# Performance work log

Hardware: AMD Instinct MI355X
Metric: run time of the kernel (lower is better)

## Reference

```python
import jax, jax.numpy as jnp
import numpy as np

NL = 2    # num_layers
H = 4     # attention heads
C = 512   # hidden_dim
IN = 256  # in_dim
F = 16    # fanout
B = 256   # seed nodes
NC = 47   # num_classes
DH = C // H
EPS = 1e-5


def _ln(x, g, b):
    mu = jnp.mean(x, -1, keepdims=True)
    var = jnp.mean((x - mu) ** 2, -1, keepdims=True)
    return (x - mu) * jax.lax.rsqrt(var + EPS) * g + b


def _mha(x, wqkv, bqkv, wo, bo):
    # torch nn.MultiheadAttention with a single batch of N tokens
    n = x.shape[0]
    qkv = x @ wqkv.T + bqkv                      # [N, 3C]
    q, k, v = jnp.split(qkv, 3, axis=-1)
    q = q.reshape(n, H, DH).transpose(1, 0, 2)   # [H, N, DH]
    k = k.reshape(n, H, DH).transpose(1, 0, 2)
    v = v.reshape(n, H, DH).transpose(1, 0, 2)
    s = jnp.einsum('hnd,hmd->hnm', q, k) * (1.0 / float(np.sqrt(DH)))
    a = jax.nn.softmax(s, axis=-1)
    o = jnp.einsum('hnm,hmd->hnd', a, v).transpose(1, 0, 2).reshape(n, C)
    return o @ wo.T + bo


def setup_inputs() -> dict:
    ks = jax.random.split(jax.random.key(0), 16)
    n = [B, B * F, B * F * F]
    p = lambda i, shape: jax.random.normal(ks[i], shape, jnp.float32) * 0.02
    return {
        'feats0': jax.random.normal(ks[0], (n[0], IN), jnp.float32),
        'feats1': jax.random.normal(ks[1], (n[1], IN), jnp.float32),
        'feats2': jax.random.normal(ks[2], (n[2], IN), jnp.float32),
        'nmask0': jnp.ones((n[0],), jnp.float32),
        'nmask1': jnp.ones((n[1],), jnp.float32),
        'nmask2': jnp.ones((n[2],), jnp.float32),
        'nbmask0': jax.random.randint(ks[3], (n[0], F), 0, 2, jnp.int32),
        'nbmask1': jax.random.randint(ks[4], (n[1], F), 0, 2, jnp.int32),
        'emb_w': p(5, (C, IN)), 'emb_b': jnp.zeros((C,), jnp.float32),
        'sage_w': p(6, (NL, C, 2 * C)), 'sage_b': jnp.zeros((NL, C), jnp.float32),
        'qkv_w': p(7, (NL, 3 * C, C)), 'qkv_b': jnp.zeros((NL, 3 * C), jnp.float32),
        'out_w': p(8, (NL, C, C)), 'out_b': jnp.zeros((NL, C), jnp.float32),
        'n1_g': jnp.ones((NL, C), jnp.float32), 'n1_b': jnp.zeros((NL, C), jnp.float32),
        'n2_g': jnp.ones((NL, C), jnp.float32), 'n2_b': jnp.zeros((NL, C), jnp.float32),
        'ffn_w1': p(9, (NL, 2 * C, C)), 'ffn_b1': jnp.zeros((NL, 2 * C), jnp.float32),
        'ffn_w2': p(10, (NL, C, 2 * C)), 'ffn_b2': jnp.zeros((NL, C), jnp.float32),
        'cls_w': p(11, (NC, C)), 'cls_b': jnp.zeros((NC,), jnp.float32),
    }


def reference(feats0, feats1, feats2, nmask0, nmask1, nmask2, nbmask0, nbmask1,
              emb_w, emb_b, sage_w, sage_b, qkv_w, qkv_b, out_w, out_b,
              n1_g, n1_b, n2_g, n2_b, ffn_w1, ffn_b1, ffn_w2, ffn_b2, cls_w, cls_b):
    nmasks = [nmask0, nmask1, nmask2]
    nbm = [nbmask0.astype(jnp.float32), nbmask1.astype(jnp.float32)]
    # embedding + node-mask gating per depth
    states = [(f @ emb_w.T + emb_b) * m[:, None]
              for f, m in zip([feats0, feats1, feats2], nmasks)]
    for li in range(NL):
        prev = states
        nxt = list(prev)
        for depth in range(NL - li - 1, -1, -1):
            # masked mean aggregation of sampled neighbors: [n_d, F, C] -> [n_d, C]
            child = prev[depth + 1].reshape(-1, F, C)
            m = nbm[depth][:, :, None]
            summed = jnp.sum(child * m, axis=1)
            denom = jnp.clip(jnp.sum(m, axis=1), 1.0)
            agg = summed / denom
            sf = prev[depth]
            # GraphSAGE concat update (no activation, dropout=0)
            h_local = jnp.concatenate([sf, agg], -1) @ sage_w[li].T + sage_b[li]
            h = _ln(sf + h_local, n1_g[li], n1_b[li])
            h = _ln(h + _mha(h, qkv_w[li], qkv_b[li], out_w[li], out_b[li]),
                    n2_g[li], n2_b[li])
            hf = jax.nn.relu(h @ ffn_w1[li].T + ffn_b1[li]) @ ffn_w2[li].T + ffn_b2[li]
            nxt[depth] = (h + hf) * nmasks[depth][:, None]
        states = nxt
    return states[0] @ cls_w.T + cls_b
```

## Files before the change

kernel.cpp:

```cpp
#include <hip/hip_runtime.h>
#include <math.h>


typedef unsigned short bf16_t;
typedef __attribute__((ext_vector_type(8))) short bf16x8_t;
typedef __attribute__((ext_vector_type(4))) float f32x4_t;

#define M_BIG 4096
#define M_CAT 4352
#define NSPLIT 4

__device__ __forceinline__ bf16_t f2bf(float f) {
  union { float f; unsigned u; } v; v.f = f;
  unsigned r = v.u + 0x7FFFu + ((v.u >> 16) & 1u);
  return (bf16_t)(r >> 16);
}
__device__ __forceinline__ float bf2f(bf16_t u) {
  union { unsigned u; float f; } v; v.u = ((unsigned)u) << 16; return v.f;
}
__device__ __forceinline__ unsigned cvtpk(float lo, float hi) {
  unsigned r;
  asm("v_cvt_pk_bf16_f32 %0, %1, %2" : "=v"(r) : "v"(lo), "v"(hi));
  return r;
}
__device__ __forceinline__ void gload16(const void* g, void* l) {
  __builtin_amdgcn_global_load_lds(
      (const __attribute__((address_space(1))) unsigned int*)g,
      (__attribute__((address_space(3))) unsigned int*)l, 16, 0, 0);
}

#define QSCALE (0.08838834764831845f * 1.4426950408889634f)

template <int BM, int BN, int MODE, bool SPLIT>
__global__ __launch_bounds__(256) void mgemm(
    const bf16_t* __restrict__ A, const bf16_t* __restrict__ A2,
    const bf16_t* __restrict__ W, const float* __restrict__ bias,
    const bf16_t* __restrict__ res, const float* __restrict__ rowa,
    const float* __restrict__ rowa2, const float* __restrict__ rowb,
    const float* __restrict__ rowc,
    bf16_t* __restrict__ Cb, bf16_t* __restrict__ Vt,
    int M, int M1, int N, int K) {
  constexpr int FM = BM / 32, FN = BN / 32;
  constexpr int NCH = (BM + BN) / 16;
  constexpr int CPW = NCH / 4;
  __shared__ bf16_t lds[2][(BM + BN) * 32];
  const int t = threadIdx.x;
  const int w = t >> 6, lane = t & 63;
  const int g = lane >> 4, li = lane & 15;
  const int bm = blockIdx.x * BM, bn = blockIdx.y * BN;
  const int wr = (w >> 1) * (BM / 2), wc = (w & 1) * (BN / 2);
  f32x4_t acc[FM][FN] = {};

  auto stage = [&](int buf, int k0) {
#pragma unroll
    for (int c0 = 0; c0 < CPW; ++c0) {
      const int c = w * CPW + c0;
      const int row = c * 16 + (lane >> 2);
      const int gk = k0 + (lane & 3) * 8;
      const bf16_t* src;
      if (row < BM) {
        const int grow = bm + row;
        if (MODE == 6) {
          src = (grow < M_CAT) ? (A + (size_t)grow * K + gk)
                               : (A2 + (size_t)(grow - M_CAT) * K + gk);
        } else if (SPLIT) {
          src = (gk < 512) ? (A + (size_t)grow * 512 + gk)
                           : (A2 + (size_t)grow * 512 + (gk - 512));
        } else {
          src = A + (size_t)grow * K + gk;
        }
      } else {
        src = W + (size_t)(bn + row - BM) * K + gk;
      }
      gload16(src, &lds[buf][c * 512]);
    }
  };

  const int nk = K / 32;
  stage(0, 0);
  for (int ks = 0; ks < nk; ++ks) {
    __syncthreads();
    if (ks + 1 < nk) stage((ks + 1) & 1, (ks + 1) * 32);
    const bf16_t* As = &lds[ks & 1][0];
    const bf16_t* Bs = &lds[ks & 1][BM * 32];
    bf16x8_t af[FM], bfr[FN];
#pragma unroll
    for (int i = 0; i < FM; ++i)
      af[i] = *(const bf16x8_t*)(As + (wr + i * 16 + li) * 32 + g * 8);
#pragma unroll
    for (int j = 0; j < FN; ++j)
      bfr[j] = *(const bf16x8_t*)(Bs + (wc + j * 16 + li) * 32 + g * 8);
#pragma unroll
    for (int i = 0; i < FM; ++i)
#pragma unroll
      for (int j = 0; j < FN; ++j)
        acc[i][j] = __builtin_amdgcn_mfma_f32_16x16x32_bf16(
            af[i], bfr[j], acc[i][j], 0, 0, 0);
  }

#pragma unroll
  for (int i = 0; i < FM; ++i) {
    const int mb = bm + wr + i * 16 + g * 4;
#pragma unroll
    for (int j = 0; j < FN; ++j) {
      const int n = bn + wc + j * 16 + li;
      if (MODE == 5) {
        const float bb = bias[n];
        if (n < 512) {
#pragma unroll
          for (int r = 0; r < 4; ++r)
            Cb[(size_t)(mb + r) * 1024 + n] = f2bf((acc[i][j][r] + bb) * QSCALE);
        } else if (n < 1024) {
#pragma unroll
          for (int r = 0; r < 4; ++r)
            Cb[(size_t)(mb + r) * 1024 + n] = f2bf(acc[i][j][r] + bb);
        } else {
          ushort4 o;
          o.x = f2bf(acc[i][j][0] + bb); o.y = f2bf(acc[i][j][1] + bb);
          o.z = f2bf(acc[i][j][2] + bb); o.w = f2bf(acc[i][j][3] + bb);
          *(ushort4*)(Vt + (size_t)(n - 1024) * M + mb) = o;
        }
      } else {
#pragma unroll
        for (int r = 0; r < 4; ++r) {
          const int m = mb + r;
          const float v = acc[i][j][r];
          if (MODE == 0) Cb[(size_t)m * N + n] = f2bf(v + bias[n]);
          if (MODE == 3) Cb[(size_t)m * N + n] = f2bf(fmaxf(v + bias[n], 0.f));
          if (MODE == 4) {
            const float ra = (m < M1) ? rowa[m] : rowa2[m - M1];
            Cb[(size_t)m * N + n] =
                f2bf((v + bias[n] + bf2f(res[(size_t)m * N + n])) * ra);
          }
          if (MODE == 6) {
            float val;
            if (m < M1) val = (v + bias[n]) * rowa[m];
            else if (m < M_CAT) val = (v + bias[n]) * rowa2[m - M1];
            else {
              const int mm = m - M_CAT;
              val = (v + bias[n] * rowb[mm]) * rowc[mm];
            }
            Cb[(size_t)m * N + n] = f2bf(val);
          }
        }
      }
    }
  }
}

template <int NW, int NQC, int SPLITS>
__global__ __launch_bounds__(NW * 64) void flashT(
    const bf16_t* __restrict__ qk, const bf16_t* __restrict__ vt,
    bf16_t* __restrict__ attno, bf16_t* __restrict__ Ofb,
    float* __restrict__ Ml, int N, int VS) {
  constexpr int QB = NW * NQC * 16;
  constexpr int KCH = 16 / NW;
  __shared__ bf16_t Ks[2][64 * 128];
  __shared__ bf16_t Vs[2][128 * 64];
  __shared__ bf16_t Ps[NW][16 * 64];
  const int bid = blockIdx.x;
  const int sp = bid % SPLITS;
  const int h = (bid / SPLITS) & 3;
  const int qb = bid / (4 * SPLITS);
  const int t = threadIdx.x, w = t >> 6, lane = t & 63;
  const int g = lane >> 4, li = lane & 15;
  const int kvbase = sp * (N / SPLITS);
  const int nt = (N / SPLITS) >> 6;

  bf16x8_t qf[NQC][4];
#pragma unroll
  for (int qc = 0; qc < NQC; ++qc) {
    const bf16_t* qrow =
        qk + (size_t)(qb * QB + w * (NQC * 16) + qc * 16 + li) * 1024 + h * 128;
#pragma unroll
    for (int ks = 0; ks < 4; ++ks)
      qf[qc][ks] = *(const bf16x8_t*)(qrow + ks * 32 + g * 8);
  }

  int koff[4], voff[2], pwoff[4];
#pragma unroll
  for (int ks = 0; ks < 4; ++ks)
    koff[ks] = li * 256 + (((ks * 4 + g) ^ (li & 7)) << 4);
#pragma unroll
  for (int ks = 0; ks < 2; ++ks)
    voff[ks] = li * 128 + (((ks * 4 + g) ^ (li & 7)) << 4);
#pragma unroll
  for (int mf = 0; mf < 4; ++mf)
    pwoff[mf] = li * 128 + (((mf * 2 + (g >> 1)) ^ (li & 7)) << 4) +
                ((g & 1) << 3);
  char* Pb = (char*)Ps + w * 2048;

  const bf16_t* kp[KCH];
  const bf16_t* vp[KCH];
#pragma unroll
  for (int i = 0; i < KCH; ++i) {
    const int c = w * KCH + i;
    const int rk = c * 4 + (lane >> 4);
    kp[i] = qk + (size_t)(kvbase + rk) * 1024 + 512 + h * 128 +
            (((lane & 15) ^ (rk & 7)) * 8);
    const int rv = c * 8 + (lane >> 3);
    vp[i] = vt + (size_t)(h * 128 + rv) * VS + kvbase +
            (((lane & 7) ^ (rv & 7)) * 8);
  }
  auto stage = [&](int buf) {
#pragma unroll
    for (int i = 0; i < KCH; ++i) {
      const int c = w * KCH + i;
      gload16(kp[i], &Ks[buf][c * 512]);
      kp[i] += (size_t)64 * 1024;
      gload16(vp[i], &Vs[buf][c * 512]);
      vp[i] += 64;
    }
  };

  f32x4_t acc[NQC][8] = {};
  float mrun[NQC], lrun[NQC];
#pragma unroll
  for (int qc = 0; qc < NQC; ++qc) { mrun[qc] = -1e30f; lrun[qc] = 0.f; }

  stage(0);
  for (int tt = 0; tt < nt; ++tt) {
    const int cur = tt & 1;
    __syncthreads();
    if (tt + 1 < nt) stage(cur ^ 1);
    const char* Kb = (const char*)Ks + cur * 16384;
    const char* Vb = (const char*)Vs + cur * 16384;

    f32x4_t sf[NQC][4];
#pragma unroll
    for (int qc = 0; qc < NQC; ++qc)
#pragma unroll
      for (int mf = 0; mf < 4; ++mf) sf[qc][mf] = (f32x4_t){0.f, 0.f, 0.f, 0.f};
    __builtin_amdgcn_s_setprio(1);
#pragma unroll
    for (int ks = 0; ks < 4; ++ks) {
#pragma unroll
      for (int mf = 0; mf < 4; ++mf) {
        const bf16x8_t kf = *(const bf16x8_t*)(Kb + koff[ks] + mf * 4096);
#pragma unroll
        for (int qc = 0; qc < NQC; ++qc)
          sf[qc][mf] = __builtin_amdgcn_mfma_f32_16x16x32_bf16(
              kf, qf[qc][ks], sf[qc][mf], 0, 0, 0);
      }
    }
    __builtin_amdgcn_s_setprio(0);

    float tmax[NQC];
#pragma unroll
    for (int qc = 0; qc < NQC; ++qc) {
      float tm = -1e30f;
#pragma unroll
      for (int mf = 0; mf < 4; ++mf)
#pragma unroll
        for (int r = 0; r < 4; ++r) tm = fmaxf(tm, sf[qc][mf][r]);
      tm = fmaxf(tm, __shfl_xor(tm, 16));
      tm = fmaxf(tm, __shfl_xor(tm, 32));
      tmax[qc] = tm;
    }
    float worst = tmax[0] - mrun[0];
#pragma unroll
    for (int qc = 1; qc < NQC; ++qc)
      worst = fmaxf(worst, tmax[qc] - mrun[qc]);
    if (!__all(worst <= 11.0f)) {
#pragma unroll
      for (int qc = 0; qc < NQC; ++qc) {
        const float mnew = fmaxf(mrun[qc], tmax[qc]);
        const float fsc = exp2f(mrun[qc] - mnew);
        mrun[qc] = mnew;
        lrun[qc] *= fsc;
#pragma unroll
        for (int mf = 0; mf < 8; ++mf) acc[qc][mf] *= fsc;
      }
    }
#pragma unroll
    for (int qc = 0; qc < NQC; ++qc) {
      float lsum = 0.f;
#pragma unroll
      for (int mf = 0; mf < 4; ++mf)
#pragma unroll
        for (int r = 0; r < 4; ++r) {
          const float p = exp2f(sf[qc][mf][r] - mrun[qc]);
          sf[qc][mf][r] = p;
          lsum += p;
        }
      lsum += __shfl_xor(lsum, 16);
      lsum += __shfl_xor(lsum, 32);
      lrun[qc] += lsum;
    }

    __builtin_amdgcn_s_setprio(1);
#pragma unroll
    for (int qc = 0; qc < NQC; ++qc) {
#pragma unroll
      for (int mf = 0; mf < 4; ++mf) {
        uint2 pv;
        pv.x = cvtpk(sf[qc][mf][0], sf[qc][mf][1]);
        pv.y = cvtpk(sf[qc][mf][2], sf[qc][mf][3]);
        *(uint2*)(Pb + pwoff[mf]) = pv;
      }
#pragma unroll
      for (int ks = 0; ks < 2; ++ks) {
        const bf16x8_t pf = *(const bf16x8_t*)(Pb + voff[ks]);
#pragma unroll
        for (int mf = 0; mf < 8; ++mf) {
          const bf16x8_t vf = *(const bf16x8_t*)(Vb + voff[ks] + mf * 2048);
          acc[qc][mf] = __builtin_amdgcn_mfma_f32_16x16x32_bf16(
              vf, pf, acc[qc][mf], 0, 0, 0);
        }
      }
    }
    __builtin_amdgcn_s_setprio(0);
  }

#pragma unroll
  for (int qc = 0; qc < NQC; ++qc) {
    const float invl = 1.f / lrun[qc];
    const int q = qb * QB + w * (NQC * 16) + qc * 16 + li;
    bf16_t* dst = (SPLITS == 1) ? (attno + (size_t)q * 512 + h * 128)
                                : (Ofb + ((size_t)sp * N + q) * 512 + h * 128);
#pragma unroll
    for (int mf = 0; mf < 8; ++mf) {
      ushort4 o;
      o.x = f2bf(acc[qc][mf][0] * invl); o.y = f2bf(acc[qc][mf][1] * invl);
      o.z = f2bf(acc[qc][mf][2] * invl); o.w = f2bf(acc[qc][mf][3] * invl);
      *(ushort4*)(dst + mf * 16 + g * 4) = o;
    }
    if (SPLITS > 1 && lane < 16) {
      float2 ml; ml.x = mrun[qc]; ml.y = lrun[qc];
      *(float2*)(Ml + ((size_t)(sp * 4 + h) * N + q) * 2) = ml;
    }
  }
}

template <int SPLITS>
__global__ __launch_bounds__(256) void merge_attn(
    const bf16_t* __restrict__ Ofb, const float* __restrict__ Ml,
    bf16_t* __restrict__ attno, int N) {
  const int q = blockIdx.x, t = threadIdx.x;
#pragma unroll
  for (int half = 0; half < 2; ++half) {
    const int c = t + half * 256;
    const int h = c >> 7;
    float2 ml[SPLITS];
    float m = -1e30f;
#pragma unroll
    for (int s = 0; s < SPLITS; ++s) {
      ml[s] = ((const float2*)Ml)[(s * 4 + h) * N + q];
      m = fmaxf(m, ml[s].x);
    }
    float num = 0.f, den = 0.f;
#pragma unroll
    for (int s = 0; s < SPLITS; ++s) {
      const float wgt = ml[s].y * exp2f(ml[s].x - m);
      num += bf2f(Ofb[((size_t)s * N + q) * 512 + c]) * wgt;
      den += wgt;
    }
    attno[(size_t)q * 512 + c] = f2bf(num / den);
  }
}

__global__ __launch_bounds__(256) void add_ln(
    const bf16_t* __restrict__ X, const bf16_t* __restrict__ Y,
    const float* __restrict__ gg, const float* __restrict__ bb,
    bf16_t* __restrict__ out) {
  const int row = blockIdx.x, t = threadIdx.x;
  const size_t base = (size_t)row * 512;
  const float x0 = bf2f(X[base + t]) + bf2f(Y[base + t]);
  const float x1 = bf2f(X[base + 256 + t]) + bf2f(Y[base + 256 + t]);
  float s = x0 + x1, ss = x0 * x0 + x1 * x1;
#pragma unroll
  for (int o = 32; o > 0; o >>= 1) {
    s += __shfl_down(s, o);
    ss += __shfl_down(ss, o);
  }
  __shared__ float rs[4], rss[4], sm[2];
  const int wv = t >> 6, ln = t & 63;
  if (ln == 0) { rs[wv] = s; rss[wv] = ss; }
  __syncthreads();
  if (t == 0) {
    const float S = rs[0] + rs[1] + rs[2] + rs[3];
    const float SS = rss[0] + rss[1] + rss[2] + rss[3];
    const float mean = S * (1.f / 512.f);
    sm[0] = mean;
    sm[1] = rsqrtf(SS * (1.f / 512.f) - mean * mean + 1e-5f);
  }
  __syncthreads();
  const float mean = sm[0], rstd = sm[1];
  out[base + t] = f2bf((x0 - mean) * rstd * gg[t] + bb[t]);
  out[base + 256 + t] = f2bf((x1 - mean) * rstd * gg[t + 256] + bb[t + 256]);
}

__global__ __launch_bounds__(256) void agg_feats(
    const float* __restrict__ feats2, const int* __restrict__ nbm,
    const float* __restrict__ nm2, bf16_t* __restrict__ aggF,
    float* __restrict__ sw, float* __restrict__ invd) {
  const int node = blockIdx.x * 4 + (threadIdx.x >> 6);
  const int lane = threadIdx.x & 63;
  float4 acc = {0.f, 0.f, 0.f, 0.f};
  float ws = 0.f, nbs = 0.f;
#pragma unroll
  for (int j = 0; j < 16; ++j) {
    const float nb = (float)nbm[node * 16 + j];
    const float wj = nb * nm2[node * 16 + j];
    const float4 v =
        *(const float4*)(feats2 + (size_t)(node * 16 + j) * 256 + lane * 4);
    acc.x += wj * v.x; acc.y += wj * v.y;
    acc.z += wj * v.z; acc.w += wj * v.w;
    ws += wj;
    nbs += nb;
  }
  ushort4 o;
  o.x = f2bf(acc.x); o.y = f2bf(acc.y); o.z = f2bf(acc.z); o.w = f2bf(acc.w);
  *(ushort4*)(aggF + (size_t)node * 256 + lane * 4) = o;
  if (lane == 0) { sw[node] = ws; invd[node] = 1.f / fmaxf(nbs, 1.f); }
}

__global__ __launch_bounds__(256) void agg_state(
    const bf16_t* __restrict__ src, const int* __restrict__ nbm,
    bf16_t* __restrict__ agg) {
  const int node = blockIdx.x * 4 + (threadIdx.x >> 6);
  const int lane = threadIdx.x & 63;
  float acc[8] = {};
  float nbs = 0.f;
#pragma unroll
  for (int j = 0; j < 16; ++j) {
    const float nb = (float)nbm[node * 16 + j];
    nbs += nb;
    const bf16x8_t v =
        *(const bf16x8_t*)(src + (size_t)(node * 16 + j) * 512 + lane * 8);
#pragma unroll
    for (int e = 0; e < 8; ++e) acc[e] += nb * bf2f((bf16_t)v[e]);
  }
  const float inv = 1.f / fmaxf(nbs, 1.f);
  bf16x8_t o;
#pragma unroll
  for (int e = 0; e < 8; ++e) o[e] = (short)f2bf(acc[e] * inv);
  *(bf16x8_t*)(agg + (size_t)node * 512 + lane * 8) = o;
}

__global__ __launch_bounds__(256) void cvt_all(
    const float* __restrict__ s_emb, const float* __restrict__ s_sage,
    const float* __restrict__ s_qkv, const float* __restrict__ s_out,
    const float* __restrict__ s_f1, const float* __restrict__ s_f2,
    const float* __restrict__ s_ft0, const float* __restrict__ s_ft1,
    bf16_t* __restrict__ d_emb, bf16_t* __restrict__ d_sage,
    bf16_t* __restrict__ d_qkv, bf16_t* __restrict__ d_out,
    bf16_t* __restrict__ d_f1, bf16_t* __restrict__ d_f2,
    bf16_t* __restrict__ d_ft0, bf16_t* __restrict__ d_ft1) {
  int i = blockIdx.x * 256 + threadIdx.x;
  const float* s; bf16_t* d; int base;
  if (i < 32768)        { s = s_emb;  d = d_emb;  base = 0; }
  else if (i < 294912)  { s = s_sage; d = d_sage; base = 32768; }
  else if (i < 688128)  { s = s_qkv;  d = d_qkv;  base = 294912; }
  else if (i < 819200)  { s = s_out;  d = d_out;  base = 688128; }
  else if (i < 1081344) { s = s_f1;   d = d_f1;   base = 819200; }
  else if (i < 1343488) { s = s_f2;   d = d_f2;   base = 1081344; }
  else if (i < 1359872) { s = s_ft0;  d = d_ft0;  base = 1343488; }
  else                  { s = s_ft1;  d = d_ft1;  base = 1359872; }
  i -= base;
  const float4 v = ((const float4*)s)[i];
  ushort4 o;
  o.x = f2bf(v.x); o.y = f2bf(v.y); o.z = f2bf(v.z); o.w = f2bf(v.w);
  ((ushort4*)d)[i] = o;
}

__global__ __launch_bounds__(256) void cls_k(
    const bf16_t* __restrict__ s, const float* __restrict__ wc,
    const float* __restrict__ bc, float* __restrict__ out) {
  __shared__ float srow[512];
  const int m = blockIdx.x, t = threadIdx.x;
  srow[t] = bf2f(s[(size_t)m * 512 + t]);
  srow[t + 256] = bf2f(s[(size_t)m * 512 + 256 + t]);
  __syncthreads();
  if (t < 47) {
    float a = bc[t];
    const float* wr = wc + (size_t)t * 512;
    for (int k = 0; k < 512; ++k) a += srow[k] * wr[k];
    out[(size_t)m * 47 + t] = a;
  }
}

extern "C" void kernel_launch(void* const* d_in, const int* in_sizes, int n_in,
                              void* d_out, int out_size, void* d_ws,
                              size_t ws_size, hipStream_t stream) {
  const float* feats0 = (const float*)d_in[0];
  const float* feats1 = (const float*)d_in[1];
  const float* feats2 = (const float*)d_in[2];
  const float* nmask0 = (const float*)d_in[3];
  const float* nmask1 = (const float*)d_in[4];
  const float* nmask2 = (const float*)d_in[5];
  const int* nbmask0 = (const int*)d_in[6];
  const int* nbmask1 = (const int*)d_in[7];
  const float* emb_w = (const float*)d_in[8];
  const float* emb_b = (const float*)d_in[9];
  const float* sage_w = (const float*)d_in[10];
  const float* sage_b = (const float*)d_in[11];
  const float* qkv_w = (const float*)d_in[12];
  const float* qkv_b = (const float*)d_in[13];
  const float* out_w = (const float*)d_in[14];
  const float* out_b = (const float*)d_in[15];
  const float* n1_g = (const float*)d_in[16];
  const float* n1_b = (const float*)d_in[17];
  const float* n2_g = (const float*)d_in[18];
  const float* n2_b = (const float*)d_in[19];
  const float* ffn_w1 = (const float*)d_in[20];
  const float* ffn_b1 = (const float*)d_in[21];
  const float* ffn_w2 = (const float*)d_in[22];
  const float* ffn_b2 = (const float*)d_in[23];
  const float* cls_w = (const float*)d_in[24];
  const float* cls_b = (const float*)d_in[25];
  float* out = (float*)d_out;

  size_t off = 0;
  auto alloc = [&](size_t bytes) {
    void* r = (char*)d_ws + off;
    off += (bytes + 255) & ~(size_t)255;
    return r;
  };
  bf16_t* wemb = (bf16_t*)alloc((size_t)512 * 256 * 2);
  bf16_t* wsage = (bf16_t*)alloc((size_t)2 * 512 * 1024 * 2);
  bf16_t* wqkv = (bf16_t*)alloc((size_t)2 * 1536 * 512 * 2);
  bf16_t* wout = (bf16_t*)alloc((size_t)2 * 512 * 512 * 2);
  bf16_t* wf1 = (bf16_t*)alloc((size_t)2 * 1024 * 512 * 2);
  bf16_t* wf2 = (bf16_t*)alloc((size_t)2 * 512 * 1024 * 2);
  bf16_t* fcat = (bf16_t*)alloc((size_t)M_CAT * 256 * 2);
  bf16_t* s_cat = (bf16_t*)alloc((size_t)2 * M_CAT * 512 * 2);
  bf16_t* agg_cat = s_cat + (size_t)M_CAT * 512;
  bf16_t* scat_o = (bf16_t*)alloc((size_t)M_CAT * 512 * 2);
  bf16_t* aggFb = (bf16_t*)alloc((size_t)4096 * 256 * 2);
  float* swv = (float*)alloc((size_t)4096 * 4);
  float* invd = (float*)alloc((size_t)4096 * 4);
  bf16_t* agg256 = (bf16_t*)alloc((size_t)256 * 512 * 2);
  bf16_t* s0f = (bf16_t*)alloc((size_t)256 * 512 * 2);
  bf16_t* tmpb = (bf16_t*)alloc((size_t)M_CAT * 512 * 2);
  bf16_t* h1 = (bf16_t*)alloc((size_t)M_CAT * 512 * 2);
  bf16_t* h2 = (bf16_t*)alloc((size_t)M_CAT * 512 * 2);
  bf16_t* qkb = (bf16_t*)alloc((size_t)M_CAT * 1024 * 2);
  bf16_t* vt = (bf16_t*)alloc((size_t)512 * M_CAT * 2);
  bf16_t* attno = (bf16_t*)alloc((size_t)M_CAT * 512 * 2);
  bf16_t* f1o = (bf16_t*)alloc((size_t)M_CAT * 1024 * 2);
  bf16_t* Ofb = (bf16_t*)alloc((size_t)NSPLIT * 4096 * 512 * 2);
  float* Ml = (float*)alloc((size_t)NSPLIT * 4 * 4096 * 2 * 4);

  cvt_all<<<6336, 256, 0, stream>>>(emb_w, sage_w, qkv_w, out_w, ffn_w1,
                                    ffn_w2, feats0, feats1, wemb, wsage, wqkv,
                                    wout, wf1, wf2, fcat + (size_t)4096 * 256,
                                    fcat);

  agg_feats<<<1024, 256, 0, stream>>>(feats2, nbmask1, nmask2, aggFb, swv, invd);
  mgemm<64, 64, 6, false><<<dim3((M_CAT + M_BIG) / 64, 8), 256, 0, stream>>>(
      fcat, aggFb, wemb, emb_b, nullptr, nmask1, nmask0, swv, invd, s_cat,
      nullptr, M_CAT + M_BIG, M_BIG, 512, 256);
  agg_state<<<64, 256, 0, stream>>>(s_cat, nbmask0,
                                    agg_cat + (size_t)M_BIG * 512);

  mgemm<64, 64, 0, true><<<dim3(M_CAT / 64, 8), 256, 0, stream>>>(
      s_cat, agg_cat, wsage, sage_b, nullptr, nullptr, nullptr, nullptr,
      nullptr, tmpb, nullptr, M_CAT, 0, 512, 1024);
  add_ln<<<M_CAT, 256, 0, stream>>>(s_cat, tmpb, n1_g, n1_b, h1);
  mgemm<64, 64, 5, false><<<dim3(M_CAT / 64, 24), 256, 0, stream>>>(
      h1, nullptr, wqkv, qkv_b, nullptr, nullptr, nullptr, nullptr, nullptr,
      qkb, vt, M_CAT, 0, 1536, 512);
  flashT<8, 2, NSPLIT><<<(M_BIG / 256) * 4 * NSPLIT, 512, 0, stream>>>(
      qkb, vt, nullptr, Ofb, Ml, M_BIG, M_CAT);
  flashT<4, 1, 1><<<(256 / 64) * 4, 256, 0, stream>>>(
      qkb + (size_t)M_BIG * 1024, vt + M_BIG, attno + (size_t)M_BIG * 512,
      nullptr, nullptr, 256, M_CAT);
  merge_attn<NSPLIT><<<M_BIG, 256, 0, stream>>>(Ofb, Ml, attno, M_BIG);
  mgemm<64, 64, 0, false><<<dim3(M_CAT / 64, 8), 256, 0, stream>>>(
      attno, nullptr, wout, out_b, nullptr, nullptr, nullptr, nullptr, nullptr,
      tmpb, nullptr, M_CAT, 0, 512, 512);
  add_ln<<<M_CAT, 256, 0, stream>>>(h1, tmpb, n2_g, n2_b, h2);
  mgemm<64, 64, 3, false><<<dim3(M_CAT / 64, 16), 256, 0, stream>>>(
      h2, nullptr, wf1, ffn_b1, nullptr, nullptr, nullptr, nullptr, nullptr,
      f1o, nullptr, M_CAT, 0, 1024, 512);
  mgemm<64, 64, 4, false><<<dim3(M_CAT / 64, 8), 256, 0, stream>>>(
      f1o, nullptr, wf2, ffn_b2, h2, nmask1, nmask0, nullptr, nullptr, scat_o,
      nullptr, M_CAT, M_BIG, 512, 1024);

  const bf16_t* s1b = scat_o;
  const bf16_t* s0b = scat_o + (size_t)M_BIG * 512;
  agg_state<<<64, 256, 0, stream>>>(s1b, nbmask0, agg256);
  const bf16_t* wsage1 = wsage + 512 * 1024;
  const bf16_t* wqkv1 = wqkv + 1536 * 512;
  const bf16_t* wout1 = wout + 512 * 512;
  const bf16_t* wf11 = wf1 + 1024 * 512;
  const bf16_t* wf21 = wf2 + 512 * 1024;
  mgemm<64, 64, 0, true><<<dim3(4, 8), 256, 0, stream>>>(
      s0b, agg256, wsage1, sage_b + 512, nullptr, nullptr, nullptr, nullptr,
      nullptr, tmpb, nullptr, 256, 0, 512, 1024);
  add_ln<<<256, 256, 0, stream>>>(s0b, tmpb, n1_g + 512, n1_b + 512, h1);
  mgemm<64, 64, 5, false><<<dim3(4, 24), 256, 0, stream>>>(
      h1, nullptr, wqkv1, qkv_b + 1536, nullptr, nullptr, nullptr, nullptr,
      nullptr, qkb, vt, 256, 0, 1536, 512);
  flashT<4, 1, 1><<<(256 / 64) * 4, 256, 0, stream>>>(
      qkb, vt, attno, nullptr, nullptr, 256, 256);
  mgemm<64, 64, 0, false><<<dim3(4, 8), 256, 0, stream>>>(
      attno, nullptr, wout1, out_b + 512, nullptr, nullptr, nullptr, nullptr,
      nullptr, tmpb, nullptr, 256, 0, 512, 512);
  add_ln<<<256, 256, 0, stream>>>(h1, tmpb, n2_g + 512, n2_b + 512, h2);
  mgemm<64, 64, 3, false><<<dim3(4, 16), 256, 0, stream>>>(
      h2, nullptr, wf11, ffn_b1 + 1024, nullptr, nullptr, nullptr, nullptr,
      nullptr, f1o, nullptr, 256, 0, 1024, 512);
  mgemm<64, 64, 4, false><<<dim3(4, 8), 256, 0, stream>>>(
      f1o, nullptr, wf21, ffn_b2 + 512, h2, nmask0, nmask0, nullptr, nullptr,
      s0f, nullptr, 256, 256, 512, 1024);

  cls_k<<<256, 256, 0, stream>>>(s0f, cls_w, cls_b, out);
}
```

Baseline: 260.8 us.

## Fuse residual LayerNorm into GEMM epilogue via last-block counter; merge flash launches

Replaces the separate add_ln kernels with a new GEMM mode. Each row-tile's column blocks increment an atomic counter, and the last block to finish runs the residual add plus LayerNorm over the full 512-wide rows and writes the normalized output. It also folds the small 256-token attention into the big split-flash launch as extra blocks, removing several launches. The cost is a serialized LayerNorm tail in one block per row tile, extra fences and atomics, and a memset of the counters.

```diff
diff --git a/kernel.cpp b/kernel.cpp
--- a/kernel.cpp
+++ b/kernel.cpp
@@ -39,11 +39,13 @@
     const float* __restrict__ rowa2, const float* __restrict__ rowb,
     const float* __restrict__ rowc,
     bf16_t* __restrict__ Cb, bf16_t* __restrict__ Vt,
-    int M, int M1, int N, int K) {
+    int M, int M1, int N, int K,
+    bf16_t* __restrict__ Hout, int* __restrict__ cnt) {
   constexpr int FM = BM / 32, FN = BN / 32;
   constexpr int NCH = (BM + BN) / 16;
   constexpr int CPW = NCH / 4;
   __shared__ bf16_t lds[2][(BM + BN) * 32];
+  __shared__ int lastflag;
   const int t = threadIdx.x;
   const int w = t >> 6, lane = t & 63;
   const int g = lane >> 4, li = lane & 15;
@@ -125,7 +127,6 @@
         for (int r = 0; r < 4; ++r) {
           const int m = mb + r;
           const float v = acc[i][j][r];
-          if (MODE == 0) Cb[(size_t)m * N + n] = f2bf(v + bias[n]);
           if (MODE == 3) Cb[(size_t)m * N + n] = f2bf(fmaxf(v + bias[n], 0.f));
           if (MODE == 4) {
             const float ra = (m < M1) ? rowa[m] : rowa2[m - M1];
@@ -142,7 +143,52 @@
             }
             Cb[(size_t)m * N + n] = f2bf(val);
           }
+          if (MODE == 7) Cb[(size_t)m * N + n] = f2bf(v + bias[n]);
         }
+      }
+    }
+  }
+
+  if (MODE == 7) {
+    __threadfence();
+    __syncthreads();
+    if (t == 0)
+      lastflag = (atomicAdd(&cnt[blockIdx.x], 1) == (int)gridDim.y - 1);
+    __syncthreads();
+    if (lastflag) {
+      __threadfence();
+      float g8[8], b8[8];
+#pragma unroll
+      for (int e = 0; e < 8; ++e) {
+        g8[e] = rowa[lane * 8 + e];
+        b8[e] = rowa2[lane * 8 + e];
+      }
+      for (int rr = 0; rr < 16; ++rr) {
+        const int row = bm + w * 16 + rr;
+        const bf16x8_t xv =
+            *(const bf16x8_t*)(res + (size_t)row * 512 + lane * 8);
+        const bf16x8_t yv =
+            *(const bf16x8_t*)(Cb + (size_t)row * 512 + lane * 8);
+        float x[8];
+        float s = 0.f, ss = 0.f;
+#pragma unroll
+        for (int e = 0; e < 8; ++e) {
+          x[e] = bf2f((bf16_t)xv[e]) + bf2f((bf16_t)yv[e]);
+          s += x[e];
+          ss += x[e] * x[e];
+        }
+#pragma unroll
+        for (int o = 1; o < 64; o <<= 1) {
+          s += __shfl_xor(s, o);
+          ss += __shfl_xor(ss, o);
+        }
+        const float mean = s * (1.f / 512.f);
+        const float rstd = rsqrtf(ss * (1.f / 512.f) - mean * mean + 1e-5f);
+        bf16x8_t ov;
+#pragma unroll
+        for (int e = 0; e < 8; ++e)
+          ov[e] = (short)f2bf((x[e] - mean) * rstd * g8[e] + b8[e]);
+        *(bf16x8_t*)(Hout + (size_t)row * 512 + lane * 8) = ov;
       }
     }
   }
@@ -152,26 +198,45 @@
 __global__ __launch_bounds__(NW * 64) void flashT(
     const bf16_t* __restrict__ qk, const bf16_t* __restrict__ vt,
     bf16_t* __restrict__ attno, bf16_t* __restrict__ Ofb,
-    float* __restrict__ Ml, int N, int VS) {
+    float* __restrict__ Ml, int N, int VS,
+    const bf16_t* __restrict__ qk2, const bf16_t* __restrict__ vt2,
+    bf16_t* __restrict__ attno2, int nbig, int N2) {
   constexpr int QB = NW * NQC * 16;
   constexpr int KCH = 16 / NW;
   __shared__ bf16_t Ks[2][64 * 128];
   __shared__ bf16_t Vs[2][128 * 64];
   __shared__ bf16_t Ps[NW][16 * 64];
   const int bid = blockIdx.x;
-  const int sp = bid % SPLITS;
-  const int h = (bid / SPLITS) & 3;
-  const int qb = bid / (4 * SPLITS);
+  int sp, h, qb, kvbase, nt;
+  bool direct;
+  const bf16_t *qkB, *vtB;
+  bf16_t* attD;
+  if (bid < nbig) {
+    sp = bid % SPLITS;
+    h = (bid / SPLITS) & 3;
+    qb = bid / (4 * SPLITS);
+    qkB = qk; vtB = vt;
+    kvbase = sp * (N / SPLITS);
+    nt = (N / SPLITS) >> 6;
+    direct = (SPLITS == 1);
+    attD = attno;
+  } else {
+    const int b2 = bid - nbig;
+    sp = 0; h = b2 & 3; qb = 0;
+    qkB = qk2; vtB = vt2;
+    kvbase = 0;
+    nt = N2 >> 6;
+    direct = true;
+    attD = attno2;
+  }
   const int t = threadIdx.x, w = t >> 6, lane = t & 63;
   const int g = lane >> 4, li = lane & 15;
-  const int kvbase = sp * (N / SPLITS);
-  const int nt = (N / SPLITS) >> 6;
 
   bf16x8_t qf[NQC][4];
 #pragma unroll
   for (int qc = 0; qc < NQC; ++qc) {
     const bf16_t* qrow =
-        qk + (size_t)(qb * QB + w * (NQC * 16) + qc * 16 + li) * 1024 + h * 128;
+        qkB + (size_t)(qb * QB + w * (NQC * 16) + qc * 16 + li) * 1024 + h * 128;
 #pragma unroll
     for (int ks = 0; ks < 4; ++ks)
       qf[qc][ks] = *(const bf16x8_t*)(qrow + ks * 32 + g * 8);
@@ -196,10 +261,10 @@
   for (int i = 0; i < KCH; ++i) {
     const int c = w * KCH + i;
     const int rk = c * 4 + (lane >> 4);
-    kp[i] = qk + (size_t)(kvbase + rk) * 1024 + 512 + h * 128 +
+    kp[i] = qkB + (size_t)(kvbase + rk) * 1024 + 512 + h * 128 +
             (((lane & 15) ^ (rk & 7)) * 8);
     const int rv = c * 8 + (lane >> 3);
-    vp[i] = vt + (size_t)(h * 128 + rv) * VS + kvbase +
+    vp[i] = vtB + (size_t)(h * 128 + rv) * VS + kvbase +
             (((lane & 7) ^ (rv & 7)) * 8);
   }
   auto stage = [&](int buf) {
@@ -316,8 +381,8 @@
   for (int qc = 0; qc < NQC; ++qc) {
     const float invl = 1.f / lrun[qc];
     const int q = qb * QB + w * (NQC * 16) + qc * 16 + li;
-    bf16_t* dst = (SPLITS == 1) ? (attno + (size_t)q * 512 + h * 128)
-                                : (Ofb + ((size_t)sp * N + q) * 512 + h * 128);
+    bf16_t* dst = direct ? (attD + (size_t)q * 512 + h * 128)
+                         : (Ofb + ((size_t)sp * N + q) * 512 + h * 128);
 #pragma unroll
     for (int mf = 0; mf < 8; ++mf) {
       ushort4 o;
@@ -325,7 +390,7 @@
       o.z = f2bf(acc[qc][mf][2] * invl); o.w = f2bf(acc[qc][mf][3] * invl);
       *(ushort4*)(dst + mf * 16 + g * 4) = o;
     }
-    if (SPLITS > 1 && lane < 16) {
+    if (!direct && lane < 16) {
       float2 ml; ml.x = mrun[qc]; ml.y = lrun[qc];
       *(float2*)(Ml + ((size_t)(sp * 4 + h) * N + q) * 2) = ml;
     }
@@ -357,37 +422,6 @@
     }
     attno[(size_t)q * 512 + c] = f2bf(num / den);
   }
-}
-
-__global__ __launch_bounds__(256) void add_ln(
-    const bf16_t* __restrict__ X, const bf16_t* __restrict__ Y,
-    const float* __restrict__ gg, const float* __restrict__ bb,
-    bf16_t* __restrict__ out) {
-  const int row = blockIdx.x, t = threadIdx.x;
-  const size_t base = (size_t)row * 512;
-  const float x0 = bf2f(X[base + t]) + bf2f(Y[base + t]);
-  const float x1 = bf2f(X[base + 256 + t]) + bf2f(Y[base + 256 + t]);
-  float s = x0 + x1, ss = x0 * x0 + x1 * x1;
-#pragma unroll
-  for (int o = 32; o > 0; o >>= 1) {
-    s += __shfl_down(s, o);
-    ss += __shfl_down(ss, o);
-  }
-  __shared__ float rs[4], rss[4], sm[2];
-  const int wv = t >> 6, ln = t & 63;
-  if (ln == 0) { rs[wv] = s; rss[wv] = ss; }
-  __syncthreads();
-  if (t == 0) {
-    const float S = rs[0] + rs[1] + rs[2] + rs[3];
-    const float SS = rss[0] + rss[1] + rss[2] + rss[3];
-    const float mean = S * (1.f / 512.f);
-    sm[0] = mean;
-    sm[1] = rsqrtf(SS * (1.f / 512.f) - mean * mean + 1e-5f);
-  }
-  __syncthreads();
-  const float mean = sm[0], rstd = sm[1];
-  out[base + t] = f2bf((x0 - mean) * rstd * gg[t] + bb[t]);
-  out[base + 256 + t] = f2bf((x1 - mean) * rstd * gg[t + 256] + bb[t + 256]);
 }
 
 __global__ __launch_bounds__(256) void agg_feats(
@@ -541,6 +575,13 @@
   bf16_t* f1o = (bf16_t*)alloc((size_t)M_CAT * 1024 * 2);
   bf16_t* Ofb = (bf16_t*)alloc((size_t)NSPLIT * 4096 * 512 * 2);
   float* Ml = (float*)alloc((size_t)NSPLIT * 4 * 4096 * 2 * 4);
+  int* cnt = (int*)alloc(1024);
+  int* c0 = cnt;
+  int* c1 = cnt + 68;
+  int* c2 = cnt + 136;
+  int* c3 = cnt + 140;
+
+  hipMemsetAsync(cnt, 0, 576, stream);
 
   cvt_all<<<6336, 256, 0, stream>>>(emb_w, sage_w, qkv_w, out_w, ffn_w1,
                                     ffn_w2, feats0, feats1, wemb, wsage, wqkv,
@@ -550,33 +591,29 @@
   agg_feats<<<1024, 256, 0, stream>>>(feats2, nbmask1, nmask2, aggFb, swv, invd);
   mgemm<64, 64, 6, false><<<dim3((M_CAT + M_BIG) / 64, 8), 256, 0, stream>>>(
       fcat, aggFb, wemb, emb_b, nullptr, nmask1, nmask0, swv, invd, s_cat,
-      nullptr, M_CAT + M_BIG, M_BIG, 512, 256);
+      nullptr, M_CAT + M_BIG, M_BIG, 512, 256, nullptr, nullptr);
   agg_state<<<64, 256, 0, stream>>>(s_cat, nbmask0,
                                     agg_cat + (size_t)M_BIG * 512);
 
-  mgemm<64, 64, 0, true><<<dim3(M_CAT / 64, 8), 256, 0, stream>>>(
-      s_cat, agg_cat, wsage, sage_b, nullptr, nullptr, nullptr, nullptr,
-      nullptr, tmpb, nullptr, M_CAT, 0, 512, 1024);
-  add_ln<<<M_CAT, 256, 0, stream>>>(s_cat, tmpb, n1_g, n1_b, h1);
+  mgemm<64, 64, 7, true><<<dim3(M_CAT / 64, 8), 256, 0, stream>>>(
+      s_cat, agg_cat, wsage, sage_b, s_cat, n1_g, n1_b, nullptr, nullptr,
+      tmpb, nullptr, M_CAT, 0, 512, 1024, h1, c0);
   mgemm<64, 64, 5, false><<<dim3(M_CAT / 64, 24), 256, 0, stream>>>(
       h1, nullptr, wqkv, qkv_b, nullptr, nullptr, nullptr, nullptr, nullptr,
-      qkb, vt, M_CAT, 0, 1536, 512);
-  flashT<8, 2, NSPLIT><<<(M_BIG / 256) * 4 * NSPLIT, 512, 0, stream>>>(
-      qkb, vt, nullptr, Ofb, Ml, M_BIG, M_CAT);
-  flashT<4, 1, 1><<<(256 / 64) * 4, 256, 0, stream>>>(
-      qkb + (size_t)M_BIG * 1024, vt + M_BIG, attno + (size_t)M_BIG * 512,
-      nullptr, nullptr, 256, M_CAT);
+      qkb, vt, M_CAT, 0, 1536, 512, nullptr, nullptr);
+  flashT<8, 2, NSPLIT><<<(M_BIG / 256) * 4 * NSPLIT + 4, 512, 0, stream>>>(
+      qkb, vt, nullptr, Ofb, Ml, M_BIG, M_CAT, qkb + (size_t)M_BIG * 1024,
+      vt + M_BIG, attno + (size_t)M_BIG * 512, (M_BIG / 256) * 4 * NSPLIT, 256);
   merge_attn<NSPLIT><<<M_BIG, 256, 0, stream>>>(Ofb, Ml, attno, M_BIG);
-  mgemm<64, 64, 0, false><<<dim3(M_CAT / 64, 8), 256, 0, stream>>>(
-      attno, nullptr, wout, out_b, nullptr, nullptr, nullptr, nullptr, nullptr,
-      tmpb, nullptr, M_CAT, 0, 512, 512);
-  add_ln<<<M_CAT, 256, 0, stream>>>(h1, tmpb, n2_g, n2_b, h2);
+  mgemm<64, 64, 7, false><<<dim3(M_CAT / 64, 8), 256, 0, stream>>>(
+      attno, nullptr, wout, out_b, h1, n2_g, n2_b, nullptr, nullptr,
+      tmpb, nullptr, M_CAT, 0, 512, 512, h2, c1);
   mgemm<64, 64, 3, false><<<dim3(M_CAT / 64, 16), 256, 0, stream>>>(
       h2, nullptr, wf1, ffn_b1, nullptr, nullptr, nullptr, nullptr, nullptr,
-      f1o, nullptr, M_CAT, 0, 1024, 512);
+      f1o, nullptr, M_CAT, 0, 1024, 512, nullptr, nullptr);
   mgemm<64, 64, 4, false><<<dim3(M_CAT / 64, 8), 256, 0, stream>>>(
       f1o, nullptr, wf2, ffn_b2, h2, nmask1, nmask0, nullptr, nullptr, scat_o,
-      nullptr, M_CAT, M_BIG, 512, 1024);
+      nullptr, M_CAT, M_BIG, 512, 1024, nullptr, nullptr);
 
   const bf16_t* s1b = scat_o;
   const bf16_t* s0b = scat_o + (size_t)M_BIG * 512;
@@ -586,25 +623,24 @@
   const bf16_t* wout1 = wout + 512 * 512;
   const bf16_t* wf11 = wf1 + 1024 * 512;
   const bf16_t* wf21 = wf2 + 512 * 1024;
-  mgemm<64, 64, 0, true><<<dim3(4, 8), 256, 0, stream>>>(
-      s0b, agg256, wsage1, sage_b + 512, nullptr, nullptr, nullptr, nullptr,
-      nullptr, tmpb, nullptr, 256, 0, 512, 1024);
-  add_ln<<<256, 256, 0, stream>>>(s0b, tmpb, n1_g + 512, n1_b + 512, h1);
+  mgemm<64, 64, 7, true><<<dim3(4, 8), 256, 0, stream>>>(
+      s0b, agg256, wsage1, sage_b + 512, s0b, n1_g + 512, n1_b + 512, nullptr,
+      nullptr, tmpb, nullptr, 256, 0, 512, 1024, h1, c2);
   mgemm<64, 64, 5, false><<<dim3(4, 24), 256, 0, stream>>>(
       h1, nullptr, wqkv1, qkv_b + 1536, nullptr, nullptr, nullptr, nullptr,
-      nullptr, qkb, vt, 256, 0, 1536, 512);
+      nullptr, qkb, vt, 256, 0, 1536, 512, nullptr, nullptr);
   flashT<4, 1, 1><<<(256 / 64) * 4, 256, 0, stream>>>(
-      qkb, vt, attno, nullptr, nullptr, 256, 256);
-  mgemm<64, 64, 0, false><<<dim3(4, 8), 256, 0, stream>>>(
-      attno, nullptr, wout1, out_b + 512, nullptr, nullptr, nullptr, nullptr,
-      nullptr, tmpb, nullptr, 256, 0, 512, 512);
-  add_ln<<<256, 256, 0, stream>>>(h1, tmpb, n2_g + 512, n2_b + 512, h2);
+      qkb, vt, attno, nullptr, nullptr, 256, 256, nullptr, nullptr, nullptr,
+      (256 / 64) * 4, 0);
+  mgemm<64, 64, 7, false><<<dim3(4, 8), 256, 0, stream>>>(
+      attno, nullptr, wout1, out_b + 512, h1, n2_g + 512, n2_b + 512, nullptr,
+      nullptr, tmpb, nullptr, 256, 0, 512, 512, h2, c3);
   mgemm<64, 64, 3, false><<<dim3(4, 16), 256, 0, stream>>>(
       h2, nullptr, wf11, ffn_b1 + 1024, nullptr, nullptr, nullptr, nullptr,
-      nullptr, f1o, nullptr, 256, 0, 1024, 512);
+      nullptr, f1o, nullptr, 256, 0, 1024, 512, nullptr, nullptr);
   mgemm<64, 64, 4, false><<<dim3(4, 8), 256, 0, stream>>>(
       f1o, nullptr, wf21, ffn_b2 + 512, h2, nmask0, nmask0, nullptr, nullptr,
-      s0f, nullptr, 256, 256, 512, 1024);
+      s0f, nullptr, 256, 256, 512, 1024, nullptr, nullptr);
 
   cls_k<<<256, 256, 0, stream>>>(s0f, cls_w, cls_b, out);
 }
```

New measurement: 455.9 us. +74.8%, slower.
